# Performance work log

Measured on AMD Instinct MI355X. Metric: run time of the kernel, lower is better.

Reference implementation:

```python
import jax, jax.numpy as jnp
import numpy as np

FS = 4            # filter_size
DIV_FLOW = 20.0   # PWCNet flow scale
T = 0.5           # timestep


def _upsample4(flow, H, W):
    # nn.Upsample(scale_factor=4, mode='bilinear', align_corners=False)
    B, C = flow.shape[0], flow.shape[1]
    return jax.image.resize(flow, (B, C, H, W), method='bilinear')


def _flow_project(flow):
    """DAIN FlowProjection: forward-scatter -flow to the 4 integer neighbors of
    (x+fx, y+fy), average by hit count, fill holes with valid 4-neighbor mean."""
    B, _, H, W = flow.shape
    gx = jnp.arange(W, dtype=flow.dtype)[None, None, :]
    gy = jnp.arange(H, dtype=flow.dtype)[None, :, None]
    x2 = gx + flow[:, 0]
    y2 = gy + flow[:, 1]
    valid = (x2 >= 0) & (x2 <= W - 1) & (y2 >= 0) & (y2 <= H - 1)
    xf = jnp.floor(x2).astype(jnp.int32)
    yf = jnp.floor(y2).astype(jnp.int32)
    vfx = jnp.where(valid, -flow[:, 0], 0.0).reshape(-1)
    vfy = jnp.where(valid, -flow[:, 1], 0.0).reshape(-1)
    vc = valid.astype(flow.dtype).reshape(-1)
    boff = (jnp.arange(B, dtype=jnp.int32) * (H * W))[:, None, None]
    accx = jnp.zeros(B * H * W, flow.dtype)
    accy = jnp.zeros(B * H * W, flow.dtype)
    cnt = jnp.zeros(B * H * W, flow.dtype)
    for dy in (0, 1):
        for dx in (0, 1):
            xi = jnp.clip(xf + dx, 0, W - 1)
            yi = jnp.clip(yf + dy, 0, H - 1)
            idx = (boff + yi * W + xi).reshape(-1)
            accx = accx.at[idx].add(vfx)
            accy = accy.at[idx].add(vfy)
            cnt = cnt.at[idx].add(vc)
    cnt = cnt.reshape(B, H, W)
    avg = jnp.stack([accx.reshape(B, H, W), accy.reshape(B, H, W)], axis=1)
    avg = avg / jnp.maximum(cnt, 1.0)[:, None]
    hole = cnt <= 0                       # (B,H,W)
    ok = (~hole).astype(flow.dtype)[:, None]
    fp = jnp.pad(avg * ok, ((0, 0), (0, 0), (1, 1), (1, 1)))
    op = jnp.pad(ok, ((0, 0), (0, 0), (1, 1), (1, 1)))
    num = fp[:, :, :-2, 1:-1] + fp[:, :, 2:, 1:-1] + fp[:, :, 1:-1, :-2] + fp[:, :, 1:-1, 2:]
    den = op[:, :, :-2, 1:-1] + op[:, :, 2:, 1:-1] + op[:, :, 1:-1, :-2] + op[:, :, 1:-1, 2:]
    filled = num / jnp.maximum(den, 1.0)
    return jnp.where(hole[:, None], filled, avg)


def _filter_interp(img, flow, filt, fs):
    """DAIN FilterInterpolation: out(p) = sum_{j,i} filt[j*fs+i,p] *
    bilinear(img, p + flow + (i+1-fs/2, j+1-fs/2))."""
    B, C, H, W = img.shape
    gx = jnp.arange(W, dtype=img.dtype)[None, None, :]
    gy = jnp.arange(H, dtype=img.dtype)[None, :, None]
    x2 = jnp.clip(gx + flow[:, 0], 0.0, W - 1.0)
    y2 = jnp.clip(gy + flow[:, 1], 0.0, H - 1.0)
    xf = jnp.floor(x2).astype(jnp.int32)
    yf = jnp.floor(y2).astype(jnp.int32)
    a = (x2 - xf)[:, None]   # (B,1,H,W)
    b = (y2 - yf)[:, None]
    w00 = (1.0 - a) * (1.0 - b)
    w10 = a * (1.0 - b)
    w01 = (1.0 - a) * b
    w11 = a * b
    flat = img.reshape(B, C, H * W)

    def gather(yi, xi):
        idx = (yi * W + xi).reshape(B, 1, H * W)
        return jnp.take_along_axis(flat, idx, axis=2).reshape(B, C, H, W)

    off = 1 - fs // 2
    out = jnp.zeros_like(img)
    for j in range(fs):
        yT = jnp.clip(yf + j + off, 0, H - 1)
        yB = jnp.clip(yf + j + off + 1, 0, H - 1)
        for i in range(fs):
            xL = jnp.clip(xf + i + off, 0, W - 1)
            xR = jnp.clip(xf + i + off + 1, 0, W - 1)
            v = (w00 * gather(yT, xL) + w10 * gather(yT, xR)
                 + w01 * gather(yB, xL) + w11 * gather(yB, xR))
            out = out + v * filt[:, j * fs + i][:, None]
    return out


def setup_inputs() -> dict:
    key = jax.random.key(0)
    k = jax.random.split(key, 6)
    B, H, W = 4, 384, 512
    return {
        'input0': jax.random.uniform(k[0], (B, 3, H, W), jnp.float32),
        'input2': jax.random.uniform(k[1], (B, 3, H, W), jnp.float32),
        'flow01': jax.random.normal(k[2], (B, 2, H // 4, W // 4), jnp.float32),
        'flow10': jax.random.normal(k[3], (B, 2, H // 4, W // 4), jnp.float32),
        'filt0': jax.random.uniform(k[4], (B, FS * FS, H, W), jnp.float32),
        'filt1': jax.random.uniform(k[5], (B, FS * FS, H, W), jnp.float32),
    }


def reference(input0, input2, flow01, flow10, filt0, filt1):
    B, _, H, W = input0.shape
    scale = DIV_FLOW * T
    f01 = _upsample4(flow01 * scale, H, W)   # F_{0->2} scaled to t=0.5
    f10 = _upsample4(flow10 * scale, H, W)   # F_{2->0} scaled to t=0.5
    Ft0 = _flow_project(f01)                 # F_{t->0}
    Ft2 = _flow_project(f10)                 # F_{t->2}
    ref0 = _filter_interp(input0, Ft0, filt0, FS)
    ref2 = _filter_interp(input2, Ft2, filt1, FS)
    return 0.5 * (ref0 + ref2)
```

## Files before the change

### kernel.cpp

```cpp
#include <hip/hip_runtime.h>

#define HH 384
#define WW 512
#define NB 4
#define HWP (HH * WW)
#define NPIX (NB * HWP)
#define SH 96
#define SW 128
#define SHW (SH * SW)

#define MBOUND 24
#define BAND 6
#define NBANDS (HH / BAND)
#define NROWS (BAND + 3)
#define OV_CAP 131072

static __device__ __forceinline__ float upsample_flow_f32(const float* __restrict__ f, int y, int x) {
    float sx = __fadd_rn(__fmul_rn((float)x, 0.25f), -0.375f);
    float sy = __fadd_rn(__fmul_rn((float)y, 0.25f), -0.375f);
    float fx0 = floorf(sx), fy0 = floorf(sy);
    float wx = __fsub_rn(sx, fx0);
    float wy = __fsub_rn(sy, fy0);
    int ix = (int)fx0, iy = (int)fy0;
    int x0 = max(ix, 0), x1 = min(ix + 1, SW - 1);
    int y0 = max(iy, 0), y1 = min(iy + 1, SH - 1);
    float v00 = __fmul_rn(10.0f, f[y0 * SW + x0]);
    float v01 = __fmul_rn(10.0f, f[y0 * SW + x1]);
    float v10 = __fmul_rn(10.0f, f[y1 * SW + x0]);
    float v11 = __fmul_rn(10.0f, f[y1 * SW + x1]);
    float omx = __fsub_rn(1.0f, wx);
    float omy = __fsub_rn(1.0f, wy);
    float w00 = __fmul_rn(omx, omy);
    float w10 = __fmul_rn(wx, omy);
    float w01 = __fmul_rn(omx, wy);
    float w11 = __fmul_rn(wx, wy);
    float s = __fmul_rn(w00, v00);
    s = __fadd_rn(s, __fmul_rn(w10, v01));
    s = __fadd_rn(s, __fmul_rn(w01, v10));
    s = __fadd_rn(s, __fmul_rn(w11, v11));
    return s;
}

__global__ __launch_bounds__(256) void upsample_k(const float* __restrict__ flow01,
                                                  const float* __restrict__ flow10,
                                                  float* __restrict__ Fu, float* __restrict__ ovf) {
    int idx = blockIdx.x * blockDim.x + threadIdx.x;
    if (idx >= NPIX) return;
    int side = blockIdx.y;
    const float* flow = side ? flow10 : flow01;
    int x = idx % WW;
    int y = (idx / WW) % HH;
    int b = idx / HWP;
    const float* fp = flow + b * 2 * SHW;
    float fx = upsample_flow_f32(fp, y, x);
    float fy = upsample_flow_f32(fp + SHW, y, x);
    float* F = Fu + side * 2 * NPIX;
    F[idx] = fx;
    F[NPIX + idx] = fy;
    float x2 = __fadd_rn((float)x, fx);
    float y2 = __fadd_rn((float)y, fy);
    bool valid = (x2 >= 0.0f && x2 <= (float)(WW - 1) && y2 >= 0.0f && y2 <= (float)(HH - 1));
    bool banded = (fy >= -(float)MBOUND && fy < (float)MBOUND);
    if (valid && !banded) {
        int xf = (int)floorf(x2);
        int yf = (int)floorf(y2);
        int key = side * NPIX + b * HWP + yf * WW + xf;
        int slot = atomicAdd((int*)ovf, 1);
        if (slot >= 0 && slot < OV_CAP) {
            ((int*)ovf)[64 + slot] = key;
            ovf[64 + OV_CAP + slot] = -fx;
            ovf[64 + 2 * OV_CAP + slot] = -fy;
        }
    }
}

static __device__ __forceinline__ void box_sum_lds(const float (&acc)[3][NROWS][WW], int rbase,
                                                   int y, int x, float& ax, float& ay, float& c) {
    float wxs1 = (x == WW - 1) ? 2.0f : 1.0f;
    float wys1 = (y == HH - 1) ? 2.0f : 1.0f;
    float sx = 0.0f, sy = 0.0f, sc = 0.0f;
    #pragma unroll
    for (int j = 0; j < 2; j++) {
        int ey = y - 1 + j;
        if (ey < 0) continue;
        float wy = j ? wys1 : 1.0f;
        int rr = ey - rbase;
        #pragma unroll
        for (int i = 0; i < 2; i++) {
            int ex = x - 1 + i;
            if (ex < 0) continue;
            float w = wy * ((i ? wxs1 : 1.0f));
            sx += w * acc[0][rr][ex];
            sy += w * acc[1][rr][ex];
            sc += w * acc[2][rr][ex];
        }
    }
    ax = sx; ay = sy; c = sc;
}

__global__ __launch_bounds__(512) void row_gather_fill_k(const float* __restrict__ Fu,
                                                         const float* __restrict__ ovf,
                                                         float* __restrict__ Ft0,
                                                         float* __restrict__ Ft2) {
    __shared__ float acc[3][NROWS][WW];
    int bid = blockIdx.x;
    int slab = bid & 7;
    int side = slab >> 2;
    int b = slab & 3;
    int t0 = (bid >> 3) * BAND;
    int rbase = t0 - 2;

    const float* Fx = Fu + side * 2 * NPIX + b * HWP;
    const float* Fyp = Fx + NPIX;

    float* A = &acc[0][0][0];
    for (int k = threadIdx.x; k < 3 * NROWS * WW; k += 512) A[k] = 0.0f;
    __syncthreads();

    int sLo = max(t0 - 2 - (MBOUND - 1), 0);
    int sHi = min(t0 + BAND + MBOUND, HH - 1);
    int npairs = (sHi - sLo + 1) * 256;
    for (int k = threadIdx.x; k < npairs; k += 512) {
        int s = sLo + (k >> 8);
        int tx = k & 255;
        int rowoff = s * WW + 2 * tx;
        float2 fxv = *(const float2*)(Fx + rowoff);
        float2 fyv = *(const float2*)(Fyp + rowoff);
        float sf = (float)s;
        #pragma unroll
        for (int u = 0; u < 2; ++u) {
            int xx = 2 * tx + u;
            float fx = u ? fxv.y : fxv.x;
            float fy = u ? fyv.y : fyv.x;
            float x2 = __fadd_rn((float)xx, fx);
            float y2 = __fadd_rn(sf, fy);
            if (x2 >= 0.0f && x2 <= (float)(WW - 1) && y2 >= 0.0f && y2 <= (float)(HH - 1)
                && fy >= -(float)MBOUND && fy < (float)MBOUND) {
                int yf = (int)floorf(y2);
                int r = yf - rbase;
                if (r >= 0 && r < NROWS) {
                    int xf = (int)floorf(x2);
                    atomicAdd(&acc[0][r][xf], -fx);
                    atomicAdd(&acc[1][r][xf], -fy);
                    atomicAdd(&acc[2][r][xf], 1.0f);
                }
            }
        }
    }

    int n = ((const int*)ovf)[0];
    n = (n < 0) ? 0 : ((n > OV_CAP) ? OV_CAP : n);
    int lo = max(rbase, 0) * WW;
    int hi = (min(t0 + BAND, HH - 1) + 1) * WW;
    int keybase = side * NPIX + b * HWP;
    for (int i = threadIdx.x; i < n; i += 512) {
        int rel = ((const int*)ovf)[64 + i] - keybase;
        if (rel >= lo && rel < hi) {
            int r = rel / WW - rbase;
            int xf = rel % WW;
            atomicAdd(&acc[0][r][xf], ovf[64 + OV_CAP + i]);
            atomicAdd(&acc[1][r][xf], ovf[64 + 2 * OV_CAP + i]);
            atomicAdd(&acc[2][r][xf], 1.0f);
        }
    }
    __syncthreads();

    float* Ft = side ? Ft2 : Ft0;
    for (int k = threadIdx.x; k < BAND * WW; k += 512) {
        int y = t0 + k / WW;
        int x = k % WW;
        float ax, ay, c;
        box_sum_lds(acc, rbase, y, x, ax, ay, c);
        float fx, fy;
        if (c > 0.0f) {
            fx = ax / c;
            fy = ay / c;
        } else {
            float nx = 0.0f, ny = 0.0f, den = 0.0f;
            float bx, by, bc;
            if (y > 0)      { box_sum_lds(acc, rbase, y - 1, x, bx, by, bc); if (bc > 0.0f) { nx += bx / bc; ny += by / bc; den += 1.0f; } }
            if (y < HH - 1) { box_sum_lds(acc, rbase, y + 1, x, bx, by, bc); if (bc > 0.0f) { nx += bx / bc; ny += by / bc; den += 1.0f; } }
            if (x > 0)      { box_sum_lds(acc, rbase, y, x - 1, bx, by, bc); if (bc > 0.0f) { nx += bx / bc; ny += by / bc; den += 1.0f; } }
            if (x < WW - 1) { box_sum_lds(acc, rbase, y, x + 1, bx, by, bc); if (bc > 0.0f) { nx += bx / bc; ny += by / bc; den += 1.0f; } }
            float inv = 1.0f / fmaxf(den, 1.0f);
            fx = nx * inv;
            fy = ny * inv;
        }
        int o = b * HWP + y * WW + x;
        Ft[o] = fx;
        Ft[NPIX + o] = fy;
    }
}

__global__ __launch_bounds__(256) void interp_k(const float* __restrict__ img0,
                                                const float* __restrict__ img2,
                                                const float* __restrict__ filt0,
                                                const float* __restrict__ filt1,
                                                const float* __restrict__ Ft0,
                                                const float* __restrict__ Ft2,
                                                float* __restrict__ out) {
    int x = blockIdx.x * 64 + threadIdx.x;
    int y = blockIdx.y * 4 + threadIdx.y;
    int bz = blockIdx.z;
    int side = bz >> 2;
    int b = bz & 3;
    const float* img  = side ? img2  : img0;
    const float* filt = side ? filt1 : filt0;
    const float* Ft   = side ? Ft2   : Ft0;

    int idx = b * HWP + y * WW + x;
    float fx = Ft[idx];
    float fy = Ft[NPIX + idx];
    float x2 = fminf(fmaxf((float)x + fx, 0.0f), (float)(WW - 1));
    float y2 = fminf(fmaxf((float)y + fy, 0.0f), (float)(HH - 1));
    float xff = floorf(x2), yff = floorf(y2);
    int xf = (int)xff, yf = (int)yff;
    float a  = x2 - xff;
    float bb = y2 - yff;
    float w00 = (1.0f - a) * (1.0f - bb);
    float w10 = a * (1.0f - bb);
    float w01 = (1.0f - a) * bb;
    float w11 = a * bb;

    float F[4][4];
    #pragma unroll
    for (int k = 0; k < 16; k++) {
        F[k >> 2][k & 3] = filt[((b * 16 + k) * HH + y) * WW + x];
    }
    float Cf[5][5];
    #pragma unroll
    for (int r = 0; r < 5; r++) {
        #pragma unroll
        for (int sc = 0; sc < 5; sc++) {
            float v = 0.0f;
            if (r < 4 && sc < 4)   v += w00 * F[r][sc];
            if (r < 4 && sc >= 1)  v += w10 * F[r][sc - 1];
            if (r >= 1 && sc < 4)  v += w01 * F[r - 1][sc];
            if (r >= 1 && sc >= 1) v += w11 * F[r - 1][sc - 1];
            Cf[r][sc] = v;
        }
    }
    int rows[5];
    #pragma unroll
    for (int r = 0; r < 5; r++) rows[r] = min(max(yf - 1 + r, 0), HH - 1);

    bool interior = (xf >= 1) && (xf <= WW - 4);
    if (interior) {
        int x0 = xf - 1;
        #pragma unroll
        for (int c = 0; c < 3; c++) {
            const float* ip = img + (b * 3 + c) * HWP;
            float accv = 0.0f;
            #pragma unroll
            for (int r = 0; r < 5; r++) {
                const float* rp = ip + rows[r] * WW + x0;
                float wrow[5];
                __builtin_memcpy(wrow, rp, 5 * sizeof(float));
                #pragma unroll
                for (int sc = 0; sc < 5; sc++) {
                    accv += Cf[r][sc] * wrow[sc];
                }
            }
            unsafeAtomicAdd(&out[((b * 3 + c) * HH + y) * WW + x], 0.5f * accv);
        }
    } else {
        int cols[5];
        #pragma unroll
        for (int sc = 0; sc < 5; sc++) cols[sc] = min(max(xf - 1 + sc, 0), WW - 1);
        #pragma unroll
        for (int c = 0; c < 3; c++) {
            const float* ip = img + (b * 3 + c) * HWP;
            float accv = 0.0f;
            #pragma unroll
            for (int r = 0; r < 5; r++) {
                const float* rp = ip + rows[r] * WW;
                #pragma unroll
                for (int sc = 0; sc < 5; sc++) {
                    accv += Cf[r][sc] * rp[cols[sc]];
                }
            }
            unsafeAtomicAdd(&out[((b * 3 + c) * HH + y) * WW + x], 0.5f * accv);
        }
    }
}

extern "C" void kernel_launch(void* const* d_in, const int* in_sizes, int n_in,
                              void* d_out, int out_size, void* d_ws, size_t ws_size,
                              hipStream_t stream) {
    const float* input0 = (const float*)d_in[0];
    const float* input2 = (const float*)d_in[1];
    const float* flow01 = (const float*)d_in[2];
    const float* flow10 = (const float*)d_in[3];
    const float* filt0  = (const float*)d_in[4];
    const float* filt1  = (const float*)d_in[5];
    float* out = (float*)d_out;

    float* ws = (float*)d_ws;
    float* Fu   = ws;
    float* Ft0  = ws + 4 * NPIX;
    float* Ft2  = ws + 6 * NPIX;
    float* ovf  = out;

    const int BS = 256;
    const int NBLK = (NPIX + BS - 1) / BS;

    hipMemsetAsync(ovf, 0, 256, stream);

    upsample_k<<<dim3(NBLK, 2), BS, 0, stream>>>(flow01, flow10, Fu, ovf);
    row_gather_fill_k<<<dim3(2 * NB * NBANDS), 512, 0, stream>>>(Fu, ovf, Ft0, Ft2);
    hipMemsetAsync(out, 0, (size_t)3 * NPIX * sizeof(float), stream);
    interp_k<<<dim3(WW / 64, HH / 4, NB * 2), dim3(64, 4), 0, stream>>>(
        input0, input2, filt0, filt1, Ft0, Ft2, out);
}
```

Baseline: 258.9 us.

## Fuse flow projection gather/fill with filter interpolation into one kernel

```diff
diff --git a/kernel.cpp b/kernel.cpp
--- a/kernel.cpp
+++ b/kernel.cpp
@@ -98,10 +98,13 @@
     ax = sx; ay = sy; c = sc;
 }
 
-__global__ __launch_bounds__(512) void row_gather_fill_k(const float* __restrict__ Fu,
-                                                         const float* __restrict__ ovf,
-                                                         float* __restrict__ Ft0,
-                                                         float* __restrict__ Ft2) {
+__global__ __launch_bounds__(512) void rgf_interp_k(const float* __restrict__ Fu,
+                                                    const float* __restrict__ ovf,
+                                                    const float* __restrict__ img0,
+                                                    const float* __restrict__ img2,
+                                                    const float* __restrict__ filt0,
+                                                    const float* __restrict__ filt1,
+                                                    float* __restrict__ out) {
     __shared__ float acc[3][NROWS][WW];
     int bid = blockIdx.x;
     int slab = bid & 7;
@@ -165,10 +168,13 @@
     }
     __syncthreads();
 
-    float* Ft = side ? Ft2 : Ft0;
-    for (int k = threadIdx.x; k < BAND * WW; k += 512) {
-        int y = t0 + k / WW;
-        int x = k % WW;
+    const float* img  = side ? img2  : img0;
+    const float* filt = side ? filt1 : filt0;
+    int x = threadIdx.x;
+
+    for (int j = 0; j < BAND; ++j) {
+        int y = t0 + j;
+
         float ax, ay, c;
         box_sum_lds(acc, rbase, y, x, ax, ay, c);
         float fx, fy;
@@ -186,100 +192,77 @@
             fx = nx * inv;
             fy = ny * inv;
         }
-        int o = b * HWP + y * WW + x;
-        Ft[o] = fx;
-        Ft[NPIX + o] = fy;
-    }
-}
-
-__global__ __launch_bounds__(256) void interp_k(const float* __restrict__ img0,
-                                                const float* __restrict__ img2,
-                                                const float* __restrict__ filt0,
-                                                const float* __restrict__ filt1,
-                                                const float* __restrict__ Ft0,
-                                                const float* __restrict__ Ft2,
-                                                float* __restrict__ out) {
-    int x = blockIdx.x * 64 + threadIdx.x;
-    int y = blockIdx.y * 4 + threadIdx.y;
-    int bz = blockIdx.z;
-    int side = bz >> 2;
-    int b = bz & 3;
-    const float* img  = side ? img2  : img0;
-    const float* filt = side ? filt1 : filt0;
-    const float* Ft   = side ? Ft2   : Ft0;
-
-    int idx = b * HWP + y * WW + x;
-    float fx = Ft[idx];
-    float fy = Ft[NPIX + idx];
-    float x2 = fminf(fmaxf((float)x + fx, 0.0f), (float)(WW - 1));
-    float y2 = fminf(fmaxf((float)y + fy, 0.0f), (float)(HH - 1));
-    float xff = floorf(x2), yff = floorf(y2);
-    int xf = (int)xff, yf = (int)yff;
-    float a  = x2 - xff;
-    float bb = y2 - yff;
-    float w00 = (1.0f - a) * (1.0f - bb);
-    float w10 = a * (1.0f - bb);
-    float w01 = (1.0f - a) * bb;
-    float w11 = a * bb;
-
-    float F[4][4];
-    #pragma unroll
-    for (int k = 0; k < 16; k++) {
-        F[k >> 2][k & 3] = filt[((b * 16 + k) * HH + y) * WW + x];
-    }
-    float Cf[5][5];
-    #pragma unroll
-    for (int r = 0; r < 5; r++) {
-        #pragma unroll
-        for (int sc = 0; sc < 5; sc++) {
-            float v = 0.0f;
-            if (r < 4 && sc < 4)   v += w00 * F[r][sc];
-            if (r < 4 && sc >= 1)  v += w10 * F[r][sc - 1];
-            if (r >= 1 && sc < 4)  v += w01 * F[r - 1][sc];
-            if (r >= 1 && sc >= 1) v += w11 * F[r - 1][sc - 1];
-            Cf[r][sc] = v;
-        }
-    }
-    int rows[5];
-    #pragma unroll
-    for (int r = 0; r < 5; r++) rows[r] = min(max(yf - 1 + r, 0), HH - 1);
-
-    bool interior = (xf >= 1) && (xf <= WW - 4);
-    if (interior) {
-        int x0 = xf - 1;
-        #pragma unroll
-        for (int c = 0; c < 3; c++) {
-            const float* ip = img + (b * 3 + c) * HWP;
-            float accv = 0.0f;
-            #pragma unroll
-            for (int r = 0; r < 5; r++) {
-                const float* rp = ip + rows[r] * WW + x0;
-                float wrow[5];
-                __builtin_memcpy(wrow, rp, 5 * sizeof(float));
+
+        float x2 = fminf(fmaxf((float)x + fx, 0.0f), (float)(WW - 1));
+        float y2 = fminf(fmaxf((float)y + fy, 0.0f), (float)(HH - 1));
+        float xff = floorf(x2), yff = floorf(y2);
+        int xf = (int)xff, yf = (int)yff;
+        float a  = x2 - xff;
+        float bb = y2 - yff;
+        float w00 = (1.0f - a) * (1.0f - bb);
+        float w10 = a * (1.0f - bb);
+        float w01 = (1.0f - a) * bb;
+        float w11 = a * bb;
+
+        float F[4][4];
+        #pragma unroll
+        for (int k = 0; k < 16; k++) {
+            F[k >> 2][k & 3] = filt[((b * 16 + k) * HH + y) * WW + x];
+        }
+        float Cf[5][5];
+        #pragma unroll
+        for (int r = 0; r < 5; r++) {
+            #pragma unroll
+            for (int sc = 0; sc < 5; sc++) {
+                float v = 0.0f;
+                if (r < 4 && sc < 4)   v += w00 * F[r][sc];
+                if (r < 4 && sc >= 1)  v += w10 * F[r][sc - 1];
+                if (r >= 1 && sc < 4)  v += w01 * F[r - 1][sc];
+                if (r >= 1 && sc >= 1) v += w11 * F[r - 1][sc - 1];
+                Cf[r][sc] = v;
+            }
+        }
+        int rows[5];
+        #pragma unroll
+        for (int r = 0; r < 5; r++) rows[r] = min(max(yf - 1 + r, 0), HH - 1);
+
+        bool interior = (xf >= 1) && (xf <= WW - 4);
+        if (interior) {
+            int x0 = xf - 1;
+            #pragma unroll
+            for (int ch = 0; ch < 3; ch++) {
+                const float* ip = img + (b * 3 + ch) * HWP;
+                float accv = 0.0f;
                 #pragma unroll
-                for (int sc = 0; sc < 5; sc++) {
-                    accv += Cf[r][sc] * wrow[sc];
+                for (int r = 0; r < 5; r++) {
+                    const float* rp = ip + rows[r] * WW + x0;
+                    float wrow[5];
+                    __builtin_memcpy(wrow, rp, 5 * sizeof(float));
+                    #pragma unroll
+                    for (int sc = 0; sc < 5; sc++) {
+                        accv += Cf[r][sc] * wrow[sc];
+                    }
                 }
-            }
-            unsafeAtomicAdd(&out[((b * 3 + c) * HH + y) * WW + x], 0.5f * accv);
-        }
-    } else {
-        int cols[5];
-        #pragma unroll
-        for (int sc = 0; sc < 5; sc++) cols[sc] = min(max(xf - 1 + sc, 0), WW - 1);
-        #pragma unroll
-        for (int c = 0; c < 3; c++) {
-            const float* ip = img + (b * 3 + c) * HWP;
-            float accv = 0.0f;
-            #pragma unroll
-            for (int r = 0; r < 5; r++) {
-                const float* rp = ip + rows[r] * WW;
+                unsafeAtomicAdd(&out[((b * 3 + ch) * HH + y) * WW + x], 0.5f * accv);
+            }
+        } else {
+            int cols[5];
+            #pragma unroll
+            for (int sc = 0; sc < 5; sc++) cols[sc] = min(max(xf - 1 + sc, 0), WW - 1);
+            #pragma unroll
+            for (int ch = 0; ch < 3; ch++) {
+                const float* ip = img + (b * 3 + ch) * HWP;
+                float accv = 0.0f;
                 #pragma unroll
-                for (int sc = 0; sc < 5; sc++) {
-                    accv += Cf[r][sc] * rp[cols[sc]];
+                for (int r = 0; r < 5; r++) {
+                    const float* rp = ip + rows[r] * WW;
+                    #pragma unroll
+                    for (int sc = 0; sc < 5; sc++) {
+                        accv += Cf[r][sc] * rp[cols[sc]];
+                    }
                 }
-            }
-            unsafeAtomicAdd(&out[((b * 3 + c) * HH + y) * WW + x], 0.5f * accv);
+                unsafeAtomicAdd(&out[((b * 3 + ch) * HH + y) * WW + x], 0.5f * accv);
+            }
         }
     }
 }
@@ -297,18 +280,15 @@
 
     float* ws = (float*)d_ws;
     float* Fu   = ws;
-    float* Ft0  = ws + 4 * NPIX;
-    float* Ft2  = ws + 6 * NPIX;
-    float* ovf  = out;
+    float* ovf  = ws + 4 * NPIX;
 
     const int BS = 256;
     const int NBLK = (NPIX + BS - 1) / BS;
 
+    hipMemsetAsync(out, 0, (size_t)3 * NPIX * sizeof(float), stream);
     hipMemsetAsync(ovf, 0, 256, stream);
 
     upsample_k<<<dim3(NBLK, 2), BS, 0, stream>>>(flow01, flow10, Fu, ovf);
-    row_gather_fill_k<<<dim3(2 * NB * NBANDS), 512, 0, stream>>>(Fu, ovf, Ft0, Ft2);
-    hipMemsetAsync(out, 0, (size_t)3 * NPIX * sizeof(float), stream);
-    interp_k<<<dim3(WW / 64, HH / 4, NB * 2), dim3(64, 4), 0, stream>>>(
-        input0, input2, filt0, filt1, Ft0, Ft2, out);
-}
+    rgf_interp_k<<<dim3(2 * NB * NBANDS), 512, 0, stream>>>(
+        Fu, ovf, input0, input2, filt0, filt1, out);
+}
```

Result: faster. 250.5 us (-3.2%).
